# Performance work log

Measured on AMD Instinct MI355X. Metric: run time of the kernel, lower is better.

## Reference

```python
import jax, jax.numpy as jnp
import numpy as np

B, H, W, C = 8, 256, 256, 128  # batch, grid-H, grid-W, channel width
MODES = 16
SCALE = 1.0 / (C * C)  # 1/(in_width*out_width)


def _corner_mask(h, w, f):
    # mask truncates the FIRST two axes of w_ft (as in the original code),
    # keeping the full rfft axis.
    m = np.zeros((h, w, f), dtype=np.float32)
    m[:MODES, :MODES, :] = 1.0
    m[-MODES:, :MODES, :] = 1.0
    m[:MODES, -MODES:, :] = 1.0
    m[-MODES:, -MODES:, :] = 1.0
    return jnp.asarray(m)


def setup_inputs() -> dict:
    key = jax.random.key(0)
    k1, k2 = jax.random.split(key)
    x = jax.random.normal(k1, (B, H, W, C), dtype=jnp.float32)
    w = SCALE * jax.random.uniform(k2, (H, W, C), dtype=jnp.float32)
    b = jnp.zeros((H, W, C), dtype=jnp.float32)
    return {"x": x, "w": w, "b": b}


def reference(x, w, b):
    # rfft2d over the innermost two dims (W, C), matching tf.signal.rfft2d
    x_ft = jnp.fft.rfft2(x, axes=(-2, -1))   # [B, H, W, C//2+1] complex
    w_ft = jnp.fft.rfft2(w, axes=(-2, -1))   # [H, W, C//2+1]
    b_ft = jnp.fft.rfft2(b, axes=(-2, -1))
    xw_ft = x_ft * w_ft + b_ft               # broadcast over batch
    mask = _corner_mask(*w_ft.shape)         # corners along axes (0,1)
    xw_ft = xw_ft * mask
    # irfft2d with default sizes recovers last dim = 2*(C//2+1-1) = C
    return jnp.fft.irfft2(xw_ft, axes=(-2, -1))
```

## Files before the change

kernel.cpp:

```cpp
#include <hip/hip_runtime.h>

#define TPK 512
#define TPA 1024

typedef float f4v __attribute__((ext_vector_type(4)));

__device__ __forceinline__ int br7(int k) {
  return (int)(__brev((unsigned int)k) >> 25);
}

template <int NT>
__device__ __forceinline__ void zero_fill_slab(float* __restrict__ out,
                                               int zi, int tid) {
  const int zb = zi / 224;
  const int zh = 16 + (zi - zb * 224);
  f4v* o4 = (f4v*)(out + ((size_t)(zb * 256 + zh)) * 32768);
  const f4v z = {0.f, 0.f, 0.f, 0.f};
  #pragma unroll 4
  for (int i = tid; i < 8192; i += NT)
    __builtin_nontemporal_store(z, &o4[i]);
}

__device__ __forceinline__ void fft16_pos(float* ar, float* ai) {
  constexpr float TC[4][8] = {
    {1.f, 0.f, 0.f, 0.f, 0.f, 0.f, 0.f, 0.f},
    {1.f, 0.f, 0.f, 0.f, 0.f, 0.f, 0.f, 0.f},
    {1.f, 0.70710678f, 0.f, -0.70710678f, 0.f, 0.f, 0.f, 0.f},
    {1.f, 0.92387953f, 0.70710678f, 0.38268343f, 0.f, -0.38268343f, -0.70710678f, -0.92387953f}
  };
  constexpr float TS[4][8] = {
    {0.f, 0.f, 0.f, 0.f, 0.f, 0.f, 0.f, 0.f},
    {0.f, 1.f, 0.f, 0.f, 0.f, 0.f, 0.f, 0.f},
    {0.f, 0.70710678f, 1.f, 0.70710678f, 0.f, 0.f, 0.f, 0.f},
    {0.f, 0.38268343f, 0.70710678f, 0.92387953f, 1.f, 0.92387953f, 0.70710678f, 0.38268343f}
  };
  #pragma unroll
  for (int s = 0; s < 4; ++s) {
    const int L = 1 << s;
    #pragma unroll
    for (int jj = 0; jj < 8; ++jj) {
      if (jj < L) {
        const float tc = TC[s][jj], ts = TS[s][jj];
        #pragma unroll
        for (int i0 = jj; i0 < 16; i0 += 2 * L) {
          const float xr = ar[i0 + L], xi = ai[i0 + L];
          const float pr = xr * tc - xi * ts;
          const float pi = xr * ts + xi * tc;
          const float qr = ar[i0], qi = ai[i0];
          ar[i0 + L] = qr - pr; ai[i0 + L] = qi - pi;
          ar[i0]     = qr + pr; ai[i0]     = qi + pi;
        }
      }
    }
  }
}

template <int TPBv>
__device__ void forward_slab(const float* __restrict__ src,
                             float (*XR)[128], float (*XI)[128],
                             float (*SR)[128], float (*SI)[128],
                             const float* Rc, const float* Rs, int tid) {
  constexpr int NQ = TPBv / 128;
  constexpr int JN = 16 / NQ;
  const int c = tid & 127;
  const int q = tid >> 7;

  constexpr float C16[16] = {1.f, 0.92387953f, 0.70710678f, 0.38268343f, 0.f,
                             -0.38268343f, -0.70710678f, -0.92387953f, -1.f,
                             -0.92387953f, -0.70710678f, -0.38268343f, 0.f,
                             0.38268343f, 0.70710678f, 0.92387953f};
  constexpr float S16[16] = {0.f, 0.38268343f, 0.70710678f, 0.92387953f, 1.f,
                             0.92387953f, 0.70710678f, 0.38268343f, 0.f,
                             -0.38268343f, -0.70710678f, -0.92387953f, -1.f,
                             -0.92387953f, -0.70710678f, -0.38268343f};

  float accR[17], accI[17];
  #pragma unroll
  for (int f = 0; f < 17; ++f) { accR[f] = 0.f; accI[f] = 0.f; }

  #pragma unroll
  for (int j = 0; j < JN; ++j) {
    const int w0 = q * JN + j;
    float xv[16];
    #pragma unroll
    for (int w1 = 0; w1 < 16; ++w1)
      xv[w1] = src[(w1 * 16 + w0) * 128 + c];
    float SRe[9], SIm[9];
    #pragma unroll
    for (int g = 0; g < 9; ++g) {
      float sr = 0.f, si = 0.f;
      #pragma unroll
      for (int w1 = 0; w1 < 16; ++w1) {
        const int m = (g * w1) & 15;
        sr = fmaf(xv[w1], C16[m], sr);
        si = fmaf(xv[w1], -S16[m], si);
      }
      SRe[g] = sr; SIm[g] = si;
    }
    #pragma unroll
    for (int f = 0; f < 17; ++f) {
      const int g = f & 15;
      const float sr = (g <= 8) ? SRe[g] : SRe[16 - g];
      const float si = (g <= 8) ? SIm[g] : -SIm[16 - g];
      const int idx = (f * w0) & 255;
      const float tc = Rc[idx], ts = -Rs[idx];
      accR[f] = fmaf(sr, tc, fmaf(-si, ts, accR[f]));
      accI[f] = fmaf(sr, ts, fmaf(si, tc, accI[f]));
    }
  }
  #pragma unroll
  for (int r = 0; r < NQ / 2; ++r) {
    if (q == 2 * r) {
      if (r == 0) {
        #pragma unroll
        for (int f = 0; f < 17; ++f) { XR[f][c] = accR[f]; XI[f][c] = accI[f]; }
      } else {
        #pragma unroll
        for (int f = 0; f < 17; ++f) { XR[f][c] += accR[f]; XI[f][c] += accI[f]; }
      }
    } else if (q == 2 * r + 1) {
      if (r == 0) {
        #pragma unroll
        for (int f = 0; f < 17; ++f) { SR[f][c] = accR[f]; SI[f][c] = accI[f]; }
      } else {
        #pragma unroll
        for (int f = 0; f < 17; ++f) { SR[f][c] += accR[f]; SI[f][c] += accI[f]; }
      }
    }
    __syncthreads();
  }
  for (int u = tid; u < 17 * 128; u += TPBv) {
    const int row = u >> 7, cc = u & 127;
    XR[row][cc] += SR[row][cc];
    XI[row][cc] += SI[row][cc];
  }
  __syncthreads();

  for (int s = 6; s >= 0; --s) {
    const int L = 1 << s;
    for (int u = tid; u < 17 * 64; u += TPBv) {
      const int row = u >> 6, qq = u & 63;
      const int jj = qq & (L - 1);
      const int pos = ((qq >> s) << (s + 1)) | jj;
      const int ti = jj << (7 - s);
      const float tc = Rc[ti], ts = Rs[ti];
      const float a0r = XR[row][pos],     a0i = XI[row][pos];
      const float b0r = XR[row][pos + L], b0i = XI[row][pos + L];
      XR[row][pos] = a0r + b0r; XI[row][pos] = a0i + b0i;
      const float dr = a0r - b0r, di = a0i - b0i;
      XR[row][pos + L] = fmaf(dr, tc, di * ts);
      XI[row][pos + L] = fmaf(di, tc, -dr * ts);
    }
    __syncthreads();
  }
}

__global__ __launch_bounds__(TPK) void k0_wft_and_fill(
    const float* __restrict__ wp, const float* __restrict__ bp,
    float2* __restrict__ wsW, float2* __restrict__ wsB,
    float* __restrict__ out) {
  const int bid = blockIdx.x;
  const int tid = threadIdx.x;
  if (bid >= 64) {
    zero_fill_slab<TPK>(out, bid - 64, tid);
    return;
  }
  __shared__ float XR[17][128], XI[17][128];
  __shared__ float SR[17][128], SI[17][128];
  __shared__ float Rc[256], Rs[256];
  for (int i = tid; i < 256; i += TPK) {
    float sv, cv; sincosf(6.283185307179586f * (float)i / 256.0f, &sv, &cv);
    Rc[i] = cv; Rs[i] = sv;
  }
  __syncthreads();
  const int which = bid >> 5;
  const int ha = bid & 31;
  const int h = (ha < 16) ? ha : (224 + ha);
  const float* src = (which ? bp : wp) + (size_t)h * 32768;
  forward_slab<TPK>(src, XR, XI, SR, SI, Rc, Rs, tid);
  float2* dst = which ? wsB : wsW;
  for (int u = tid; u < 32 * 65; u += TPK) {
    const int fi = u / 65, k = u - fi * 65;
    const int f = fi - 16;
    float xr, xi;
    if (f >= 0) { const int p = br7(k); xr = XR[f][p]; xi = XI[f][p]; }
    else { const int kk = (128 - k) & 127; const int p = br7(kk);
           xr = XR[-f][p]; xi = -XI[-f][p]; }
    dst[(ha * 32 + fi) * 65 + k] = make_float2(xr, xi);
  }
}

__global__ __launch_bounds__(TPA) void fourier_active(
    const float* __restrict__ x, const float2* __restrict__ wsW,
    const float2* __restrict__ wsB, float* __restrict__ out) {
  const int bid = blockIdx.x;
  const int tid = threadIdx.x;
  __shared__ float XR[17][128], XI[17][128];
  __shared__ float TR[32][128], TI[32][128];
  __shared__ float Rc[256], Rs[256];
  for (int i = tid; i < 256; i += TPA) {
    float sv, cv; sincosf(6.283185307179586f * (float)i / 256.0f, &sv, &cv);
    Rc[i] = cv; Rs[i] = sv;
  }
  __syncthreads();

  const int b = bid >> 5;
  const int ha = bid & 31;
  const int h = (ha < 16) ? ha : (224 + ha);
  const float* src = x + ((size_t)(b * 256 + h)) * 32768;
  forward_slab<TPA>(src, XR, XI, (float(*)[128])TR, (float(*)[128])TI,
                    Rc, Rs, tid);

  for (int u = tid; u < 32 * 128; u += TPA) {
    const int fi = u >> 7, k = u & 127;
    float gr = 0.f, gi = 0.f;
    if (k <= 64) {
      const int f = fi - 16;
      float xr, xi;
      if (f >= 0) { const int p = br7(k); xr = XR[f][p]; xi = XI[f][p]; }
      else { const int kk = (128 - k) & 127; const int p = br7(kk);
             xr = XR[-f][p]; xi = -XI[-f][p]; }
      const float2 wf = wsW[(ha * 32 + fi) * 65 + k];
      const float2 bf = wsB[(ha * 32 + fi) * 65 + k];
      gr = xr * wf.x - xi * wf.y + bf.x;
      gi = xr * wf.y + xi * wf.x + bf.y;
      const float al = (k == 0 || k == 64) ? 1.f : 2.f;
      gr *= al; gi *= al;
    }
    const int p = br7(k);
    TR[fi][p] = gr; TI[fi][p] = gi;
  }
  __syncthreads();

  for (int s = 0; s <= 6; ++s) {
    const int L = 1 << s;
    for (int u = tid; u < 32 * 64; u += TPA) {
      const int row = u >> 6, qq = u & 63;
      const int jj = qq & (L - 1);
      const int pos = ((qq >> s) << (s + 1)) | jj;
      const int ti = jj << (7 - s);
      const float tc = Rc[ti], ts = Rs[ti];
      const float b0r = TR[row][pos + L], b0i = TI[row][pos + L];
      const float pr = b0r * tc - b0i * ts;
      const float pi = fmaf(b0r, ts, b0i * tc);
      const float a0r = TR[row][pos], a0i = TI[row][pos];
      TR[row][pos + L] = a0r - pr; TI[row][pos + L] = a0i - pi;
      TR[row][pos]     = a0r + pr; TI[row][pos]     = a0i + pi;
    }
    __syncthreads();
  }

  const int c = tid & 127;
  const int q = tid >> 7;
  constexpr int BR4[16] = {0, 8, 4, 12, 2, 10, 6, 14, 1, 9, 5, 13, 3, 11, 7, 15};
  const float inv = 1.0f / 32768.0f;
  float* og = out + ((size_t)(b * 256 + h)) * 32768;

  #pragma unroll 1
  for (int it = 0; it < 2; ++it) {
    const int w0 = q + it * 8;
    float Ur[16], Ui[16];
    #pragma unroll
    for (int g = 0; g < 16; ++g) {
      const int gb = BR4[g];
      const float t1r = TR[gb + 16][c], t1i = TI[gb + 16][c];
      const float t0r = TR[gb][c],      t0i = TI[gb][c];
      const int i1 = (gb * w0) & 255;
      const int i2 = ((gb - 16) * w0) & 255;
      const float c1 = Rc[i1], s1 = Rs[i1];
      const float c2 = Rc[i2], s2 = Rs[i2];
      Ur[g] = t1r * c1 - t1i * s1 + t0r * c2 - t0i * s2;
      Ui[g] = t1r * s1 + t1i * c1 + t0r * s2 + t0i * c2;
    }
    fft16_pos(Ur, Ui);
    #pragma unroll
    for (int w1 = 0; w1 < 16; ++w1)
      og[(w1 * 16 + w0) * 128 + c] = Ur[w1] * inv;
  }
}

extern "C" void kernel_launch(void* const* d_in, const int* in_sizes, int n_in,
                              void* d_out, int out_size, void* d_ws, size_t ws_size,
                              hipStream_t stream) {
  const float* x = (const float*)d_in[0];
  const float* w = (const float*)d_in[1];
  const float* b = (const float*)d_in[2];
  float* out = (float*)d_out;
  float2* wsW = (float2*)d_ws;
  float2* wsB = wsW + 32 * 32 * 65;

  hipLaunchKernelGGL(k0_wft_and_fill, dim3(64 + 1792), dim3(TPK), 0, stream,
                     w, b, wsW, wsB, out);
  hipLaunchKernelGGL(fourier_active, dim3(256), dim3(TPA), 0, stream,
                     x, wsW, wsB, out);
}
```

Baseline: 73.29 us.

## Split active-slab pipeline into two kernels and spread zero-fill across all launches

The fused active kernel is split into a forward-reduction kernel that writes intermediate spectra to workspace and a second kernel that finishes the FFT, multiplies, and inverts. The zero-filling of the inactive output rows, previously all done in the first kernel, is now spread across the three launches so it can overlap the compute blocks. Block size drops from 1024 to 512 threads in the active kernels, and the zero-fill loop is fully unrolled. The cost is an extra launch and a global round trip for the intermediate data.

Result: slower. 80.45 us (+9.8%).

```diff
diff --git a/kernel.cpp b/kernel.cpp
--- a/kernel.cpp
+++ b/kernel.cpp
@@ -1,7 +1,9 @@
 #include <hip/hip_runtime.h>
 
-#define TPK 512
-#define TPA 1024
+#define TPB 512
+#define NF_K0 448
+#define NF_KA 640
+#define NF_KB 704
 
 typedef float f4v __attribute__((ext_vector_type(4)));
 
@@ -16,9 +18,9 @@
   const int zh = 16 + (zi - zb * 224);
   f4v* o4 = (f4v*)(out + ((size_t)(zb * 256 + zh)) * 32768);
   const f4v z = {0.f, 0.f, 0.f, 0.f};
-  #pragma unroll 4
-  for (int i = tid; i < 8192; i += NT)
-    __builtin_nontemporal_store(z, &o4[i]);
+  #pragma unroll
+  for (int i = 0; i < 8192 / NT; ++i)
+    __builtin_nontemporal_store(z, &o4[tid + i * NT]);
 }
 
 __device__ __forceinline__ void fft16_pos(float* ar, float* ai) {
@@ -56,10 +58,10 @@
 }
 
 template <int TPBv>
-__device__ void forward_slab(const float* __restrict__ src,
-                             float (*XR)[128], float (*XI)[128],
-                             float (*SR)[128], float (*SI)[128],
-                             const float* Rc, const float* Rs, int tid) {
+__device__ void phaseA_reduce(const float* __restrict__ src,
+                              float (*XR)[128], float (*XI)[128],
+                              float (*SR)[128], float (*SI)[128],
+                              const float* Rc, const float* Rs, int tid) {
   constexpr int NQ = TPBv / 128;
   constexpr int JN = 16 / NQ;
   const int c = tid & 127;
@@ -135,7 +137,11 @@
     XI[row][cc] += SI[row][cc];
   }
   __syncthreads();
-
+}
+
+template <int TPBv>
+__device__ void fftc17_lds(float (*XR)[128], float (*XI)[128],
+                           const float* Rc, const float* Rs, int tid) {
   for (int s = 6; s >= 0; --s) {
     const int L = 1 << s;
     for (int u = tid; u < 17 * 64; u += TPBv) {
@@ -155,20 +161,20 @@
   }
 }
 
-__global__ __launch_bounds__(TPK) void k0_wft_and_fill(
+__global__ __launch_bounds__(TPB) void k0_wft_and_fill(
     const float* __restrict__ wp, const float* __restrict__ bp,
     float2* __restrict__ wsW, float2* __restrict__ wsB,
     float* __restrict__ out) {
   const int bid = blockIdx.x;
   const int tid = threadIdx.x;
   if (bid >= 64) {
-    zero_fill_slab<TPK>(out, bid - 64, tid);
+    zero_fill_slab<TPB>(out, bid - 64, tid);
     return;
   }
   __shared__ float XR[17][128], XI[17][128];
   __shared__ float SR[17][128], SI[17][128];
   __shared__ float Rc[256], Rs[256];
-  for (int i = tid; i < 256; i += TPK) {
+  for (int i = tid; i < 256; i += TPB) {
     float sv, cv; sincosf(6.283185307179586f * (float)i / 256.0f, &sv, &cv);
     Rc[i] = cv; Rs[i] = sv;
   }
@@ -177,9 +183,10 @@
   const int ha = bid & 31;
   const int h = (ha < 16) ? ha : (224 + ha);
   const float* src = (which ? bp : wp) + (size_t)h * 32768;
-  forward_slab<TPK>(src, XR, XI, SR, SI, Rc, Rs, tid);
+  phaseA_reduce<TPB>(src, XR, XI, SR, SI, Rc, Rs, tid);
+  fftc17_lds<TPB>(XR, XI, Rc, Rs, tid);
   float2* dst = which ? wsB : wsW;
-  for (int u = tid; u < 32 * 65; u += TPK) {
+  for (int u = tid; u < 32 * 65; u += TPB) {
     const int fi = u / 65, k = u - fi * 65;
     const int f = fi - 16;
     float xr, xi;
@@ -190,28 +197,65 @@
   }
 }
 
-__global__ __launch_bounds__(TPA) void fourier_active(
-    const float* __restrict__ x, const float2* __restrict__ wsW,
+__global__ __launch_bounds__(TPB) void ka_phaseA(
+    const float* __restrict__ x, float2* __restrict__ Xs,
+    float* __restrict__ out) {
+  const int bid = blockIdx.x;
+  const int tid = threadIdx.x;
+  if (bid >= 256) {
+    zero_fill_slab<TPB>(out, NF_K0 + (bid - 256), tid);
+    return;
+  }
+  __shared__ float XR[17][128], XI[17][128];
+  __shared__ float SR[17][128], SI[17][128];
+  __shared__ float Rc[256], Rs[256];
+  for (int i = tid; i < 256; i += TPB) {
+    float sv, cv; sincosf(6.283185307179586f * (float)i / 256.0f, &sv, &cv);
+    Rc[i] = cv; Rs[i] = sv;
+  }
+  __syncthreads();
+  const int slab = bid;
+  const int b = slab >> 5;
+  const int ha = slab & 31;
+  const int h = (ha < 16) ? ha : (224 + ha);
+  const float* src = x + ((size_t)(b * 256 + h)) * 32768;
+  phaseA_reduce<TPB>(src, XR, XI, SR, SI, Rc, Rs, tid);
+  float2* dst = Xs + (size_t)slab * 2176;
+  for (int u = tid; u < 17 * 128; u += TPB)
+    dst[u] = make_float2(XR[u >> 7][u & 127], XI[u >> 7][u & 127]);
+}
+
+__global__ __launch_bounds__(TPB) void kb_rest(
+    const float2* __restrict__ Xs, const float2* __restrict__ wsW,
     const float2* __restrict__ wsB, float* __restrict__ out) {
   const int bid = blockIdx.x;
   const int tid = threadIdx.x;
+  if (bid >= 256) {
+    zero_fill_slab<TPB>(out, NF_K0 + NF_KA + (bid - 256), tid);
+    return;
+  }
   __shared__ float XR[17][128], XI[17][128];
   __shared__ float TR[32][128], TI[32][128];
   __shared__ float Rc[256], Rs[256];
-  for (int i = tid; i < 256; i += TPA) {
+  for (int i = tid; i < 256; i += TPB) {
     float sv, cv; sincosf(6.283185307179586f * (float)i / 256.0f, &sv, &cv);
     Rc[i] = cv; Rs[i] = sv;
   }
-  __syncthreads();
-
-  const int b = bid >> 5;
-  const int ha = bid & 31;
+  const int slab = bid;
+  const int b = slab >> 5;
+  const int ha = slab & 31;
   const int h = (ha < 16) ? ha : (224 + ha);
-  const float* src = x + ((size_t)(b * 256 + h)) * 32768;
-  forward_slab<TPA>(src, XR, XI, (float(*)[128])TR, (float(*)[128])TI,
-                    Rc, Rs, tid);
-
-  for (int u = tid; u < 32 * 128; u += TPA) {
+  const float2* Xp = Xs + (size_t)slab * 2176;
+  for (int u = tid; u < 17 * 128; u += TPB) {
+    const float2 v = Xp[u];
+    XR[u >> 7][u & 127] = v.x;
+    XI[u >> 7][u & 127] = v.y;
+  }
+  __syncthreads();
+
+  fftc17_lds<TPB>(XR, XI, Rc, Rs, tid);
+
+  for (int u = tid; u < 32 * 128; u += TPB) {
     const int fi = u >> 7, k = u & 127;
     float gr = 0.f, gi = 0.f;
     if (k <= 64) {
@@ -234,7 +278,7 @@
 
   for (int s = 0; s <= 6; ++s) {
     const int L = 1 << s;
-    for (int u = tid; u < 32 * 64; u += TPA) {
+    for (int u = tid; u < 32 * 64; u += TPB) {
       const int row = u >> 6, qq = u & 63;
       const int jj = qq & (L - 1);
       const int pos = ((qq >> s) << (s + 1)) | jj;
@@ -257,8 +301,8 @@
   float* og = out + ((size_t)(b * 256 + h)) * 32768;
 
   #pragma unroll 1
-  for (int it = 0; it < 2; ++it) {
-    const int w0 = q + it * 8;
+  for (int it = 0; it < 4; ++it) {
+    const int w0 = q + it * 4;
     float Ur[16], Ui[16];
     #pragma unroll
     for (int g = 0; g < 16; ++g) {
@@ -288,9 +332,12 @@
   float* out = (float*)d_out;
   float2* wsW = (float2*)d_ws;
   float2* wsB = wsW + 32 * 32 * 65;
-
-  hipLaunchKernelGGL(k0_wft_and_fill, dim3(64 + 1792), dim3(TPK), 0, stream,
+  float2* Xs  = wsB + 32 * 32 * 65;
+
+  hipLaunchKernelGGL(k0_wft_and_fill, dim3(64 + NF_K0), dim3(TPB), 0, stream,
                      w, b, wsW, wsB, out);
-  hipLaunchKernelGGL(fourier_active, dim3(256), dim3(TPA), 0, stream,
-                     x, wsW, wsB, out);
-}
+  hipLaunchKernelGGL(ka_phaseA, dim3(256 + NF_KA), dim3(TPB), 0, stream,
+                     x, Xs, out);
+  hipLaunchKernelGGL(kb_rest, dim3(256 + NF_KB), dim3(TPB), 0, stream,
+                     Xs, wsW, wsB, out);
+}
```
